# Optimization experiments

Hardware: AMD Instinct MI355X
Metric: run time of the kernel (lower is better)

## Reference

```python
import jax, jax.numpy as jnp
import numpy as np

R, A, E, K, NREL = 2048, 16384, 131072, 48, 7
RADIUS = 10.0


def setup_inputs():
    key = jax.random.key(0)
    ks = jax.random.split(key, 20)
    f = jax.random.normal
    return {
        "node_feature": f(ks[0], (R, 21), jnp.float32),
        "all_atom_pos": f(ks[1], (A, 3), jnp.float32) * 8.0,
        "atom_name": jax.random.randint(ks[2], (A,), 0, 38),
        "ca_idx": jax.random.randint(ks[3], (R,), 0, A),
        "edge_src": jax.random.randint(ks[4], (E,), 0, R),
        "edge_dst": jax.random.randint(ks[5], (E,), 0, R),
        "edge_rel": jax.random.randint(ks[6], (E,), 0, NREL),
        # parameters (atom-type embedding table, residue-type linear, AEP point MLP,
        # relational graph conv, env2structures MLP with BN)
        "emb_atom": f(ks[7], (39, 64), jnp.float32) * 0.02,
        "Wres": f(ks[8], (21, 64), jnp.float32) * 0.1,
        "bres": jnp.zeros((64,), jnp.float32),
        "Wxyz": f(ks[9], (3, 64), jnp.float32) * 0.1,
        "W1": f(ks[10], (64, 128), jnp.float32) * 0.1,
        "b1": jnp.zeros((128,), jnp.float32),
        "W2": f(ks[11], (128, 256), jnp.float32) * 0.08,
        "b2": jnp.zeros((256,), jnp.float32),
        "Wconv": f(ks[12], (NREL * 64, 512), jnp.float32) * 0.05,
        "bconv": jnp.zeros((512,), jnp.float32),
        "Wself": f(ks[13], (64, 512), jnp.float32) * 0.1,
        "We1": f(ks[14], (512 + 256, 512), jnp.float32) * 0.05,
        "be1": jnp.zeros((512,), jnp.float32),
        "gamma1": jnp.ones((512,), jnp.float32),
        "beta1": jnp.zeros((512,), jnp.float32),
        "We2": f(ks[15], (512, 512), jnp.float32) * 0.05,
        "be2": jnp.zeros((512,), jnp.float32),
    }


def reference(node_feature, all_atom_pos, atom_name, ca_idx, edge_src, edge_dst, edge_rel,
              emb_atom, Wres, bres, Wxyz, W1, b1, W2, b2,
              Wconv, bconv, Wself, We1, be1, gamma1, beta1, We2, be2):
    # residue-type embedding (nn.Linear(21, 64))
    res_feat = node_feature @ Wres + bres                      # [R,64]
    # ball query: each CA gathers all-atom neighbors within RADIUS (fixed K, masked)
    ca = all_atom_pos[ca_idx]                                   # [R,3]
    diff = ca[:, None, :] - all_atom_pos[None, :, :]            # [R,A,3]
    d = jnp.sqrt(jnp.sum(diff * diff, axis=-1) + 1e-12)         # [R,A]
    dm = jnp.where(d < RADIUS, d, jnp.inf)
    negd, nbr = jax.lax.top_k(-dm, K)                           # K nearest in ball
    mask = (-negd) < RADIUS                                     # [R,K]
    maskf = mask.astype(res_feat.dtype)[..., None]
    delta = (all_atom_pos[nbr] - ca[:, None, :]) * maskf        # relative coords [R,K,3]
    # padded atom-type embedding (padding contributes zeros, like padding_idx=38)
    pts = (emb_atom[atom_name[nbr]] + delta @ Wxyz) * maskf     # [R,K,64]
    # AEP point MLP + masked max-pool -> environment feature
    h = jax.nn.relu(pts @ W1 + b1)                              # [R,K,128]
    env = jnp.max(jnp.where(mask[..., None], h, -1e9), axis=1)  # [R,128]
    env = jax.nn.relu(env @ W2 + b2)                            # [R,256]
    # relational graph conv: per-relation scatter-sum over destination nodes
    seg = edge_dst * NREL + edge_rel
    agg = jax.ops.segment_sum(res_feat[edge_src], seg, num_segments=R * NREL)
    agg = agg.reshape(R, NREL * res_feat.shape[1])              # [R, 7*64]
    hres = jax.nn.relu(agg @ Wconv + bconv + res_feat @ Wself)  # [R,512]
    # env2structures MLP (Linear -> BatchNorm1d(train stats) -> ReLU -> Linear)
    z = jnp.concatenate([hres, env], axis=-1) @ We1 + be1       # [R,512]
    z = (z - z.mean(0)) * jax.lax.rsqrt(z.var(0) + 1e-5) * gamma1 + beta1
    return jax.nn.relu(z) @ We2 + be2                           # [R,512]
```

## Files before the change

kernel.cpp:

```cpp
#include <hip/hip_runtime.h>
#include <math.h>

#define R_ 2048
#define A_ 16384
#define E_ 131072
#define K_ 48
#define NREL_ 7

typedef __attribute__((ext_vector_type(8))) short bfrag8;
typedef __attribute__((ext_vector_type(4))) float f32x4v;

__device__ __forceinline__ unsigned short bf16rne(float f) {
    unsigned u = __builtin_bit_cast(unsigned, f);
    u += 0x7FFFu + ((u >> 16) & 1u);
    return (unsigned short)(u >> 16);
}

__device__ __forceinline__ float dist2(float x, float y, float z,
                                       float cx, float cy, float cz) {
    float dx = x - cx, dy = y - cy, dz = z - cz;
    return fmaf(dx, dx, fmaf(dy, dy, dz * dz));
}

__global__ __launch_bounds__(256) void k_prep(
    const float* __restrict__ Wconv, const float* __restrict__ Wself,
    const float* __restrict__ We1, const float* __restrict__ We2,
    const float* __restrict__ W1,
    const float* __restrict__ node, const float* __restrict__ Wres,
    const float* __restrict__ bres,
    unsigned short* __restrict__ Bt1, unsigned short* __restrict__ Bt2,
    unsigned short* __restrict__ Bt3, unsigned short* __restrict__ W1t,
    float* __restrict__ resfeat, float* __restrict__ bufA)
{
    int id = blockIdx.x * 256 + threadIdx.x;
    if (id < 262144) {
        int k = id & 511, n = id >> 9;
        float v = (k < 448) ? Wconv[k * 512 + n] : Wself[(k - 448) * 512 + n];
        Bt1[n * 512 + k] = bf16rne(v);
    } else if (id < 655360) {
        int rel = id - 262144;
        int k = rel % 768, n = rel / 768;
        Bt2[n * 768 + k] = bf16rne(We1[k * 512 + n]);
    } else if (id < 917504) {
        int rel = id - 655360;
        int k = rel & 511, n = rel >> 9;
        Bt3[n * 512 + k] = bf16rne(We2[k * 512 + n]);
    } else if (id < 925696) {
        int rel = id - 917504;
        int k = rel & 63, n = rel >> 6;
        W1t[n * 64 + k] = bf16rne(W1[k * 128 + n]);
    } else if (id < 1056768) {
        int rel = id - 925696;
        int r = rel >> 6, c = rel & 63;
        float s = bres[c];
#pragma unroll
        for (int i = 0; i < 21; ++i) s += node[r * 21 + i] * Wres[i * 64 + c];
        resfeat[r * 64 + c] = s;
        bufA[(size_t)r * 512 + 448 + c] = s;
    }
}

__global__ __launch_bounds__(256) void k_edges(
    const int* __restrict__ esrc, const int* __restrict__ edst,
    const int* __restrict__ erel, const float* __restrict__ resfeat,
    float* __restrict__ bufA)
{
    int idx = blockIdx.x * 256 + threadIdx.x;
    int e = idx >> 6, c = idx & 63;
    int d = edst[e], rel = erel[e], s = esrc[e];
    atomicAdd(&bufA[(size_t)d * 512 + rel * 64 + c], resfeat[s * 64 + c]);
}

__global__ __launch_bounds__(256) void k_ball(
    const float* __restrict__ pos, const int* __restrict__ ca_idx,
    int* __restrict__ nbr)
{
    __shared__ unsigned binsw[4096];
    __shared__ unsigned hist[256];
    __shared__ unsigned hist2[256];
    __shared__ int sc[256];
    __shared__ float candd[128];
    __shared__ int candi[128];
    __shared__ unsigned s_cnt, s_ccnt;
    __shared__ int s_list[64];
    __shared__ int sB, sNeed, sB2, sNeed2, sTotal;

    int tid = threadIdx.x;
    int r = blockIdx.x;
    int ca = ca_idx[r];
    float cx = pos[ca * 3 + 0], cy = pos[ca * 3 + 1], cz = pos[ca * 3 + 2];

    hist[tid] = 0u;
    if (tid == 0) { s_cnt = 0u; s_ccnt = 0u; }
    __syncthreads();

    for (int it = 0; it < 16; ++it) {
        int a0 = it * 1024 + tid * 4;
        const float4* p = (const float4*)(pos + (size_t)a0 * 3);
        float4 p0 = p[0], p1 = p[1], p2 = p[2];
        float xs[4] = { p0.x, p0.w, p1.z, p2.y };
        float ys[4] = { p0.y, p1.x, p1.w, p2.z };
        float zs[4] = { p0.z, p1.y, p2.x, p2.w };
        unsigned pack = 0;
#pragma unroll
        for (int q = 0; q < 4; ++q) {
            float d2 = dist2(xs[q], ys[q], zs[q], cx, cy, cz);
            int b = 255;
            if (d2 < 100.0f) {
                b = (int)(d2 * 2.56f); if (b > 254) b = 254;
                atomicAdd(&hist[b], 1u);
            }
            pack |= (unsigned)b << (q * 8);
        }
        binsw[it * 256 + tid] = pack;
    }
    __syncthreads();

    sc[tid] = (int)hist[tid];
    __syncthreads();
    for (int s = 1; s < 256; s <<= 1) {
        int v = (tid >= s) ? sc[tid - s] : 0;
        __syncthreads();
        sc[tid] += v;
        __syncthreads();
    }
    if (tid == 0) sTotal = sc[255];
    if (sc[tid] >= K_ && (tid == 0 || sc[tid - 1] < K_)) {
        sB = tid;
        sNeed = K_ - (sc[tid] - (int)hist[tid]);
    }
    __syncthreads();

    int mode = (sTotal <= K_) ? 0 : (((int)hist[sB] > 128) ? 2 : 1);

    if (mode <= 1) {
        int B = (mode == 0) ? 255 : sB;
        for (int it = 0; it < 16; ++it) {
            unsigned pack = binsw[it * 256 + tid];
            int a0 = it * 1024 + tid * 4;
#pragma unroll
            for (int q = 0; q < 4; ++q) {
                int b = (pack >> (q * 8)) & 255;
                if (b < B) { unsigned pp = atomicAdd(&s_cnt, 1u); s_list[pp] = a0 + q; }
                else if (b == B && mode == 1) {
                    unsigned c = atomicAdd(&s_ccnt, 1u);
                    if (c < 128u) candi[c] = a0 + q;
                }
            }
        }
    } else {
        int B = sB;
        float lo2 = B * 0.390625f;
        hist2[tid] = 0u;
        __syncthreads();
        for (int it = 0; it < 16; ++it) {
            unsigned pack = binsw[it * 256 + tid];
            int a0 = it * 1024 + tid * 4;
#pragma unroll
            for (int q = 0; q < 4; ++q) {
                if (((pack >> (q * 8)) & 255) == (unsigned)B) {
                    int a = a0 + q;
                    float d2 = dist2(pos[a * 3], pos[a * 3 + 1], pos[a * 3 + 2], cx, cy, cz);
                    int k2 = (int)((d2 - lo2) * 655.36f);
                    if (k2 < 0) k2 = 0; if (k2 > 255) k2 = 255;
                    atomicAdd(&hist2[k2], 1u);
                }
            }
        }
        __syncthreads();
        sc[tid] = (int)hist2[tid];
        __syncthreads();
        for (int s = 1; s < 256; s <<= 1) {
            int v = (tid >= s) ? sc[tid - s] : 0;
            __syncthreads();
            sc[tid] += v;
            __syncthreads();
        }
        if (sc[tid] >= sNeed && (tid == 0 || sc[tid - 1] < sNeed)) {
            sB2 = tid;
            sNeed2 = sNeed - (sc[tid] - (int)hist2[tid]);
        }
        __syncthreads();
        int B2 = sB2;
        for (int it = 0; it < 16; ++it) {
            unsigned pack = binsw[it * 256 + tid];
            int a0 = it * 1024 + tid * 4;
#pragma unroll
            for (int q = 0; q < 4; ++q) {
                int b = (pack >> (q * 8)) & 255;
                if (b < B) { unsigned pp = atomicAdd(&s_cnt, 1u); s_list[pp] = a0 + q; }
                else if (b == B) {
                    int a = a0 + q;
                    float d2 = dist2(pos[a * 3], pos[a * 3 + 1], pos[a * 3 + 2], cx, cy, cz);
                    int k2 = (int)((d2 - lo2) * 655.36f);
                    if (k2 < 0) k2 = 0; if (k2 > 255) k2 = 255;
                    if (k2 < B2) { unsigned pp = atomicAdd(&s_cnt, 1u); s_list[pp] = a; }
                    else if (k2 == B2) {
                        unsigned c = atomicAdd(&s_ccnt, 1u);
                        if (c < 128u) candi[c] = a;
                    }
                }
            }
        }
    }
    __syncthreads();

    int needN = (mode == 0) ? 0 : ((mode == 1) ? sNeed : sNeed2);
    unsigned C = s_ccnt; if (C > 128u) C = 128u;
    if (tid < (int)C) {
        int a = candi[tid];
        float d2 = dist2(pos[a * 3], pos[a * 3 + 1], pos[a * 3 + 2], cx, cy, cz);
        candd[tid] = sqrtf(d2 + 1e-12f);
    }
    __syncthreads();
    if (tid < (int)C) {
        float di = candd[tid]; int ii = candi[tid];
        int rank = 0;
        for (unsigned j = 0; j < C; ++j) {
            float dj = candd[j]; int ij = candi[j];
            if (dj < di || (dj == di && ij < ii)) ++rank;
        }
        if (rank < needN) { unsigned pp = atomicAdd(&s_cnt, 1u); s_list[pp] = ii; }
    }
    __syncthreads();
    if (tid < K_) nbr[r * K_ + tid] = (tid < (int)s_cnt) ? s_list[tid] : -1;
}

__global__ __launch_bounds__(256) void k_env(
    const float* __restrict__ pos, const int* __restrict__ atom_name,
    const int* __restrict__ ca_idx, const int* __restrict__ nbr,
    const float* __restrict__ emb, const float* __restrict__ Wxyz,
    const unsigned short* __restrict__ W1t,
    const float* __restrict__ b1,
    const float* __restrict__ W2, const float* __restrict__ b2,
    float* __restrict__ outZ1)
{
    __shared__ __align__(16) float pts[48 * 68];
    __shared__ __align__(16) unsigned short W1s[128 * 72];
    __shared__ float env128[128];
    __shared__ float sWxyz[192];
    __shared__ float s_d[48][3];
    __shared__ int s_a[48];
    __shared__ int s_an[48];

    int tid = threadIdx.x, r = blockIdx.x;

    for (int c = tid; c < 1024; c += 256)
        *(uint4*)((char*)W1s + (c >> 3) * 144 + (c & 7) * 16) = ((const uint4*)W1t)[c];
    if (tid < 192) sWxyz[tid] = Wxyz[tid];

    int ca = ca_idx[r];
    float cx = pos[ca * 3 + 0], cy = pos[ca * 3 + 1], cz = pos[ca * 3 + 2];
    if (tid < K_) {
        int a = nbr[r * K_ + tid];
        s_a[tid] = a;
        if (a >= 0) {
            s_d[tid][0] = pos[a * 3 + 0] - cx;
            s_d[tid][1] = pos[a * 3 + 1] - cy;
            s_d[tid][2] = pos[a * 3 + 2] - cz;
            s_an[tid] = atom_name[a];
        } else {
            s_d[tid][0] = 0.f; s_d[tid][1] = 0.f; s_d[tid][2] = 0.f;
            s_an[tid] = 0;
        }
    }
    __syncthreads();

    for (int idx = tid; idx < K_ * 64; idx += 256) {
        int row = idx >> 6, k = idx & 63;
        int a = s_a[row];
        float v = 0.f;
        if (a >= 0) {
            v = emb[s_an[row] * 64 + k]
              + s_d[row][0] * sWxyz[k] + s_d[row][1] * sWxyz[64 + k]
              + s_d[row][2] * sWxyz[128 + k];
        }
        pts[row * 68 + k] = v;
    }
    __syncthreads();

    int w = tid >> 6, l = tid & 63;
    int fr = l & 15, fo = l >> 4;
    f32x4v acc[3][2];
#pragma unroll
    for (int m = 0; m < 3; ++m)
#pragma unroll
        for (int n = 0; n < 2; ++n) acc[m][n] = (f32x4v){0.f, 0.f, 0.f, 0.f};

#pragma unroll
    for (int ks = 0; ks < 2; ++ks) {
        bfrag8 af[3], bf[2];
#pragma unroll
        for (int m = 0; m < 3; ++m) {
            int row = 16 * m + fr;
            const char* base = (const char*)pts + row * 272 + ks * 128 + fo * 32;
            float4 v0 = *(const float4*)base;
            float4 v1 = *(const float4*)(base + 16);
            bfrag8 t;
            t[0] = (short)bf16rne(v0.x); t[1] = (short)bf16rne(v0.y);
            t[2] = (short)bf16rne(v0.z); t[3] = (short)bf16rne(v0.w);
            t[4] = (short)bf16rne(v1.x); t[5] = (short)bf16rne(v1.y);
            t[6] = (short)bf16rne(v1.z); t[7] = (short)bf16rne(v1.w);
            af[m] = t;
        }
#pragma unroll
        for (int n = 0; n < 2; ++n) {
            int wrow = (2 * w + n) * 16 + fr;
            bf[n] = *(const bfrag8*)((const char*)W1s + wrow * 144 + ks * 64 + fo * 16);
        }
#pragma unroll
        for (int m = 0; m < 3; ++m)
#pragma unroll
            for (int n = 0; n < 2; ++n)
                acc[m][n] = __builtin_amdgcn_mfma_f32_16x16x32_bf16(af[m], bf[n], acc[m][n], 0, 0, 0);
    }

#pragma unroll
    for (int n = 0; n < 2; ++n) {
        int col = 32 * w + n * 16 + fr;
        float bv = b1[col];
        float m = -1e30f;
#pragma unroll
        for (int mt = 0; mt < 3; ++mt) {
#pragma unroll
            for (int i = 0; i < 4; ++i) {
                int row = 16 * mt + fo * 4 + i;
                if (s_a[row] >= 0) m = fmaxf(m, fmaxf(acc[mt][n][i] + bv, 0.f));
            }
        }
        m = fmaxf(m, __shfl_xor(m, 16));
        m = fmaxf(m, __shfl_xor(m, 32));
        if (fo == 0 && (l & 48) == 0) env128[col] = m;
    }
    __syncthreads();

    {
        float s = b2[tid];
        for (int i = 0; i < 128; ++i) s += env128[i] * W2[i * 256 + tid];
        outZ1[(size_t)r * 768 + 512 + tid] = fmaxf(s, 0.f);
    }
}

template<bool RELU_OUT, bool BN_A, bool STATS>
__global__ __launch_bounds__(256) void k_mgemm(
    const float* __restrict__ A, int lda, int K,
    const unsigned short* __restrict__ Bt,
    const float* __restrict__ bias,
    const float* __restrict__ stats, const float* __restrict__ gamma,
    const float* __restrict__ beta,
    float* __restrict__ C, int ldc, float* __restrict__ statsOut)
{
    __shared__ __align__(16) unsigned short As[32 * 32];
    __shared__ __align__(16) unsigned short Bs[64 * 32];
    __shared__ float bnsc[BN_A ? 512 : 1];
    __shared__ float bnsh[BN_A ? 512 : 1];

    int tid = threadIdx.x;
    int m0 = blockIdx.y * 32, n0 = blockIdx.x * 64;

    if (BN_A) {
        for (int i = tid; i < 512; i += 256) {
            float mean = stats[i] * (1.0f / 2048.0f);
            float var = stats[512 + i] * (1.0f / 2048.0f) - mean * mean;
            float inv = 1.0f / sqrtf(var + 1e-5f);
            float scv = gamma[i] * inv;
            bnsc[i] = scv;
            bnsh[i] = beta[i] - mean * scv;
        }
        __syncthreads();
    }

    int w = tid >> 6, l = tid & 63;
    int wm = w >> 1, wn = w & 1;

    int ar = tid >> 3, ac = tid & 7;
    int aslot = ac >> 1, ahalf = ac & 1;
    int abyte = ar * 64 + ((aslot ^ ((ar >> 1) & 3)) << 4) + ahalf * 8;
    int bn_ = tid >> 2, bs_ = tid & 3;
    int bbyte = bn_ * 64 + ((bs_ ^ ((bn_ >> 1) & 3)) << 4);

    int fr = l & 15, fo = l >> 4;
    int arow = 16 * wm + fr;
    int afbyte = arow * 64 + ((fo ^ ((arow >> 1) & 3)) << 4);
    int bcol0 = 32 * wn + fr;
    int bfbyte0 = bcol0 * 64 + ((fo ^ ((bcol0 >> 1) & 3)) << 4);
    int bcol1 = bcol0 + 16;
    int bfbyte1 = bcol1 * 64 + ((fo ^ ((bcol1 >> 1) & 3)) << 4);

    f32x4v acc0 = { 0.f, 0.f, 0.f, 0.f };
    f32x4v acc1 = { 0.f, 0.f, 0.f, 0.f };

    for (int k0 = 0; k0 < K; k0 += 32) {
        float4 av = *(const float4*)(A + (size_t)(m0 + ar) * lda + k0 + ac * 4);
        uint4 bv = *(const uint4*)(Bt + (size_t)(n0 + bn_) * K + k0 + bs_ * 8);
        if (BN_A) {
            int kb = k0 + ac * 4;
            av.x = fmaxf(av.x * bnsc[kb + 0] + bnsh[kb + 0], 0.f);
            av.y = fmaxf(av.y * bnsc[kb + 1] + bnsh[kb + 1], 0.f);
            av.z = fmaxf(av.z * bnsc[kb + 2] + bnsh[kb + 2], 0.f);
            av.w = fmaxf(av.w * bnsc[kb + 3] + bnsh[kb + 3], 0.f);
        }
        unsigned lo = (unsigned)bf16rne(av.x) | ((unsigned)bf16rne(av.y) << 16);
        unsigned hi = (unsigned)bf16rne(av.z) | ((unsigned)bf16rne(av.w) << 16);
        __syncthreads();
        *(uint2*)((char*)As + abyte) = make_uint2(lo, hi);
        *(uint4*)((char*)Bs + bbyte) = bv;
        __syncthreads();

        bfrag8 af = *(const bfrag8*)((const char*)As + afbyte);
        bfrag8 bf0 = *(const bfrag8*)((const char*)Bs + bfbyte0);
        bfrag8 bf1 = *(const bfrag8*)((const char*)Bs + bfbyte1);
        acc0 = __builtin_amdgcn_mfma_f32_16x16x32_bf16(af, bf0, acc0, 0, 0, 0);
        acc1 = __builtin_amdgcn_mfma_f32_16x16x32_bf16(af, bf1, acc1, 0, 0, 0);
    }

    int col0 = n0 + 32 * wn + fr;
    int row = m0 + 16 * wm + fo * 4;
    float bb0 = bias[col0], bb1 = bias[col0 + 16];
    float s0 = 0.f, q0 = 0.f, s1 = 0.f, q1 = 0.f;
#pragma unroll
    for (int i = 0; i < 4; ++i) {
        float v0 = acc0[i] + bb0;
        float v1 = acc1[i] + bb1;
        if (RELU_OUT) { v0 = fmaxf(v0, 0.f); v1 = fmaxf(v1, 0.f); }
        if (STATS) { s0 += v0; q0 += v0 * v0; s1 += v1; q1 += v1 * v1; }
        C[(size_t)(row + i) * ldc + col0] = v0;
        C[(size_t)(row + i) * ldc + col0 + 16] = v1;
    }
    if (STATS) {
        s0 += __shfl_xor(s0, 16); s0 += __shfl_xor(s0, 32);
        q0 += __shfl_xor(q0, 16); q0 += __shfl_xor(q0, 32);
        s1 += __shfl_xor(s1, 16); s1 += __shfl_xor(s1, 32);
        q1 += __shfl_xor(q1, 16); q1 += __shfl_xor(q1, 32);
        if (fo == 0 && (l & 48) == 0) {
            atomicAdd(&statsOut[col0], s0);
            atomicAdd(&statsOut[512 + col0], q0);
            atomicAdd(&statsOut[col0 + 16], s1);
            atomicAdd(&statsOut[512 + col0 + 16], q1);
        }
    }
}

extern "C" void kernel_launch(void* const* d_in, const int* in_sizes, int n_in,
                              void* d_out, int out_size, void* d_ws, size_t ws_size,
                              hipStream_t stream)
{
    const float* node   = (const float*)d_in[0];
    const float* pos    = (const float*)d_in[1];
    const int*   aname  = (const int*)d_in[2];
    const int*   caidx  = (const int*)d_in[3];
    const int*   esrc   = (const int*)d_in[4];
    const int*   edst   = (const int*)d_in[5];
    const int*   erel   = (const int*)d_in[6];
    const float* emb    = (const float*)d_in[7];
    const float* Wres   = (const float*)d_in[8];
    const float* bres   = (const float*)d_in[9];
    const float* Wxyz   = (const float*)d_in[10];
    const float* W1     = (const float*)d_in[11];
    const float* b1     = (const float*)d_in[12];
    const float* W2     = (const float*)d_in[13];
    const float* b2     = (const float*)d_in[14];
    const float* Wconv  = (const float*)d_in[15];
    const float* bconv  = (const float*)d_in[16];
    const float* Wself  = (const float*)d_in[17];
    const float* We1    = (const float*)d_in[18];
    const float* be1    = (const float*)d_in[19];
    const float* gamma1 = (const float*)d_in[20];
    const float* beta1  = (const float*)d_in[21];
    const float* We2    = (const float*)d_in[22];
    const float* be2    = (const float*)d_in[23];
    float* out = (float*)d_out;

    char* ws = (char*)d_ws;
    float* resfeat = (float*)(ws + 0);
    float* bufA    = (float*)(ws + 524288);
    float* bufZ1   = (float*)(ws + 4718592);
    float* bufZ2   = (float*)(ws + 11010048);
    int*   nbr     = (int*)  (ws + 15204352);
    float* stats   = (float*)(ws + 15597568);
    unsigned short* Bt1 = (unsigned short*)(ws + 15601664);
    unsigned short* Bt2 = (unsigned short*)(ws + 16125952);
    unsigned short* Bt3 = (unsigned short*)(ws + 16912384);
    unsigned short* W1t = (unsigned short*)(ws + 17436672);

    hipMemsetAsync(bufA, 0, (size_t)R_ * 512 * 4, stream);
    hipMemsetAsync(stats, 0, 1024 * 4, stream);

    k_prep<<<4128, 256, 0, stream>>>(Wconv, Wself, We1, We2, W1, node, Wres, bres,
                                     Bt1, Bt2, Bt3, W1t, resfeat, bufA);
    k_ball<<<R_, 256, 0, stream>>>(pos, caidx, nbr);
    k_env<<<R_, 256, 0, stream>>>(pos, aname, caidx, nbr, emb, Wxyz, W1t, b1, W2, b2, bufZ1);
    k_edges<<<(size_t)E_ * 64 / 256, 256, 0, stream>>>(esrc, edst, erel, resfeat, bufA);

    dim3 gg(512 / 64, R_ / 32);
    k_mgemm<true, false, false><<<gg, 256, 0, stream>>>(
        bufA, 512, 512, Bt1, bconv, nullptr, nullptr, nullptr, bufZ1, 768, nullptr);
    k_mgemm<false, false, true><<<gg, 256, 0, stream>>>(
        bufZ1, 768, 768, Bt2, be1, nullptr, nullptr, nullptr, bufZ2, 512, stats);
    k_mgemm<false, true, false><<<gg, 256, 0, stream>>>(
        bufZ2, 512, 512, Bt3, be2, stats, gamma1, beta1, out, 512, nullptr);
}
```

Baseline: 234.2 us.

## Replace atomic edge scatter-add with CSR sort and per-node gather reduction

Per-edge float atomicAdd into the relational aggregation buffer is replaced by a counting sort of edges by (dst, rel) segment: a histogram, a single-block prefix scan, and a scatter of source indices. A gather kernel then sums source features per segment in registers and writes each output once, which also removes the memset of the aggregation buffer. This is meant to cut float-atomic contention and traffic, at the cost of three extra small launches, a serial one-block scan, and integer atomics during the scatter.

After: 237.7 us. About the same (+1.5%).

```diff
diff --git a/kernel.cpp b/kernel.cpp
--- a/kernel.cpp
+++ b/kernel.cpp
@@ -60,15 +60,67 @@
     }
 }
 
-__global__ __launch_bounds__(256) void k_edges(
+__global__ __launch_bounds__(256) void k_hist(
+    const int* __restrict__ edst, const int* __restrict__ erel,
+    int* __restrict__ cnt)
+{
+    int e = blockIdx.x * 256 + threadIdx.x;
+    atomicAdd(&cnt[edst[e] * NREL_ + erel[e]], 1);
+}
+
+__global__ __launch_bounds__(1024) void k_scan(
+    const int* __restrict__ cnt, int* __restrict__ offs, int* __restrict__ cursor)
+{
+    __shared__ int part[1024];
+    int t = threadIdx.x;
+    int base = t * 14;
+    int loc[14];
+    int s = 0;
+#pragma unroll
+    for (int i = 0; i < 14; ++i) { loc[i] = s; s += cnt[base + i]; }
+    part[t] = s;
+    __syncthreads();
+    for (int st = 1; st < 1024; st <<= 1) {
+        int v = (t >= st) ? part[t - st] : 0;
+        __syncthreads();
+        part[t] += v;
+        __syncthreads();
+    }
+    int excl = (t == 0) ? 0 : part[t - 1];
+#pragma unroll
+    for (int i = 0; i < 14; ++i) {
+        int o = excl + loc[i];
+        offs[base + i] = o;
+        cursor[base + i] = o;
+    }
+    if (t == 1023) offs[14336] = part[1023];
+}
+
+__global__ __launch_bounds__(256) void k_scatter(
     const int* __restrict__ esrc, const int* __restrict__ edst,
-    const int* __restrict__ erel, const float* __restrict__ resfeat,
-    float* __restrict__ bufA)
-{
-    int idx = blockIdx.x * 256 + threadIdx.x;
-    int e = idx >> 6, c = idx & 63;
-    int d = edst[e], rel = erel[e], s = esrc[e];
-    atomicAdd(&bufA[(size_t)d * 512 + rel * 64 + c], resfeat[s * 64 + c]);
+    const int* __restrict__ erel, int* __restrict__ cursor,
+    int* __restrict__ eord)
+{
+    int e = blockIdx.x * 256 + threadIdx.x;
+    int seg = edst[e] * NREL_ + erel[e];
+    int p = atomicAdd(&cursor[seg], 1);
+    eord[p] = esrc[e];
+}
+
+__global__ __launch_bounds__(256) void k_gather(
+    const int* __restrict__ offs, const int* __restrict__ eord,
+    const float* __restrict__ resfeat, float* __restrict__ bufA)
+{
+    int r = blockIdx.x;
+    int c = threadIdx.x & 63, rg = threadIdx.x >> 6;
+    for (int rel = rg; rel < NREL_; rel += 4) {
+        int seg = r * NREL_ + rel;
+        int j0 = offs[seg], j1 = offs[seg + 1];
+        float acc = 0.f;
+        for (int j = j0; j < j1; ++j)
+            acc += resfeat[eord[j] * 64 + c];
+        bufA[(size_t)r * 512 + rel * 64 + c] = acc;
+    }
 }
 
 __global__ __launch_bounds__(256) void k_ball(
@@ -482,15 +534,23 @@
     unsigned short* Bt2 = (unsigned short*)(ws + 16125952);
     unsigned short* Bt3 = (unsigned short*)(ws + 16912384);
     unsigned short* W1t = (unsigned short*)(ws + 17436672);
-
-    hipMemsetAsync(bufA, 0, (size_t)R_ * 512 * 4, stream);
+    int* cnt    = (int*)(ws + 17453056);
+    int* offs   = (int*)(ws + 17510400);
+    int* cursor = (int*)(ws + 17567760);
+    int* eord   = (int*)(ws + 17625120);
+
+    hipMemsetAsync(cnt, 0, 14336 * 4, stream);
     hipMemsetAsync(stats, 0, 1024 * 4, stream);
+
+    k_hist<<<E_ / 256, 256, 0, stream>>>(edst, erel, cnt);
+    k_scan<<<1, 1024, 0, stream>>>(cnt, offs, cursor);
+    k_scatter<<<E_ / 256, 256, 0, stream>>>(esrc, edst, erel, cursor, eord);
 
     k_prep<<<4128, 256, 0, stream>>>(Wconv, Wself, We1, We2, W1, node, Wres, bres,
                                      Bt1, Bt2, Bt3, W1t, resfeat, bufA);
     k_ball<<<R_, 256, 0, stream>>>(pos, caidx, nbr);
     k_env<<<R_, 256, 0, stream>>>(pos, aname, caidx, nbr, emb, Wxyz, W1t, b1, W2, b2, bufZ1);
-    k_edges<<<(size_t)E_ * 64 / 256, 256, 0, stream>>>(esrc, edst, erel, resfeat, bufA);
+    k_gather<<<R_, 256, 0, stream>>>(offs, eord, resfeat, bufA);
 
     dim3 gg(512 / 64, R_ / 32);
     k_mgemm<true, false, false><<<gg, 256, 0, stream>>>(
```
